# Optimization experiments

Hardware: AMD Instinct MI355X
Metric: run time of the kernel (lower is better)

The kernel has to match this reference:

```python
import jax, jax.numpy as jnp
import numpy as np

B, S, H = 2, 2048, 2048
N_HEADS = 16
HEAD_DIM = H // N_HEADS


def setup_inputs() -> dict:
    key = jax.random.key(0)
    k1, k2, k3 = jax.random.split(key, 3)
    # Xavier-uniform-ish init for weights, zeros for biases (matches _init_weights)
    lim_in = float(np.sqrt(6.0 / (H + 3 * H)))
    lim_out = float(np.sqrt(6.0 / (H + H)))
    return {
        "hidden_states": jax.random.normal(k1, (B, S, H), dtype=jnp.float32),
        "W_in": jax.random.uniform(k2, (3 * H, H), jnp.float32, -lim_in, lim_in),
        "b_in": jnp.zeros((3 * H,), jnp.float32),
        "W_out": jax.random.uniform(k3, (H, H), jnp.float32, -lim_out, lim_out),
        "b_out": jnp.zeros((H,), jnp.float32),
    }


def reference(hidden_states, W_in, b_in, W_out, b_out):
    b, s, h = hidden_states.shape
    qkv = hidden_states @ W_in.T + b_in  # [B,S,3H]
    q, k, v = jnp.split(qkv, 3, axis=-1)
    # [B,S,H] -> [B,N,S,D]
    def to_heads(x):
        return x.reshape(b, s, N_HEADS, HEAD_DIM).transpose(0, 2, 1, 3)
    q, k, v = to_heads(q), to_heads(k), to_heads(v)
    scale = HEAD_DIM ** -0.5
    scores = jnp.einsum("bnqd,bnkd->bnqk", q, k) * scale  # [B,N,S,S]
    causal = jnp.triu(jnp.ones((s, s), dtype=bool), k=1)
    scores = jnp.where(causal, -jnp.inf, scores)
    weights = jax.nn.softmax(scores, axis=-1)
    attn = jnp.einsum("bnqk,bnkd->bnqd", weights, v)  # [B,N,S,D]
    attn = attn.transpose(0, 2, 1, 3).reshape(b, s, h)
    return attn @ W_out.T + b_out
```

## Files before the change

### kernel.cpp

```cpp
#include <hip/hip_runtime.h>
#include <cstdint>

typedef __bf16 bf16x8 __attribute__((ext_vector_type(8)));
typedef __bf16 bf16x4 __attribute__((ext_vector_type(4)));
typedef float  f32x4  __attribute__((ext_vector_type(4)));

__device__ __forceinline__ void lds_load16(const void* g, void* l) {
  __builtin_amdgcn_global_load_lds(
      (const __attribute__((address_space(1))) unsigned int*)g,
      (__attribute__((address_space(3))) unsigned int*)l, 16, 0, 0);
}

#define BAR() do { asm volatile("" ::: "memory"); __builtin_amdgcn_s_barrier(); asm volatile("" ::: "memory"); } while (0)

__device__ __forceinline__ float grp16_max(float v) {
  v = fmaxf(v, __shfl_xor(v, 1));
  v = fmaxf(v, __shfl_xor(v, 2));
  v = fmaxf(v, __shfl_xor(v, 4));
  v = fmaxf(v, __shfl_xor(v, 8));
  return v;
}
__device__ __forceinline__ float grp16_sum(float v) {
  v += __shfl_xor(v, 1);
  v += __shfl_xor(v, 2);
  v += __shfl_xor(v, 4);
  v += __shfl_xor(v, 8);
  return v;
}

__global__ void f2bf_kernel(const float* __restrict__ in, __bf16* __restrict__ out, int n4) {
  int i = blockIdx.x * blockDim.x + threadIdx.x;
  if (i >= n4) return;
  const float4 v = reinterpret_cast<const float4*>(in)[i];
  bf16x4 o;
  o[0] = (__bf16)v.x; o[1] = (__bf16)v.y; o[2] = (__bf16)v.z; o[3] = (__bf16)v.w;
  reinterpret_cast<bf16x4*>(out)[i] = o;
}

template <int EPI>
__global__ __launch_bounds__(512, 1)
void gemm256(const __bf16* __restrict__ A, const __bf16* __restrict__ Bm,
             const float* __restrict__ bias,
             __bf16* __restrict__ qo, __bf16* __restrict__ ko, __bf16* __restrict__ vo,
             float* __restrict__ co)
{
  constexpr int K = 2048, NT = K / 64;
  __shared__ __align__(16) char lds8[131072];

  const int t = threadIdx.x;
  const int lane = t & 63, w = t >> 6;
  const int g = lane >> 4, r16 = lane & 15;
  const int wm = w >> 2, wn = w & 3;

  const int bid = blockIdx.x;
  int tM, tN;
  if (EPI == 0) {
    const int swz = (bid & 7) * 48 + (bid >> 3);
    tM = (swz & 15) * 256;
    tN = (swz >> 4) * 256;
  } else {
    const int swz = (bid & 7) * 16 + (bid >> 3);
    tM = (swz & 15) * 256;
    tN = (swz >> 4) * 256;
  }

  const char* Ag = (const char*)A + (size_t)tM * K * 2;
  const char* Bg = (const char*)Bm + (size_t)tN * K * 2;
  const int ld = K * 2;

  auto STAGE_HALF = [&](int X, int h, int tb, int ktg) {
#pragma unroll
    for (int i = 0; i < 2; i++) {
      int o = i * 8192 + t * 16;
      int rl = o >> 7;
      int inrow = (o & 127) ^ ((rl & 7) << 4);
      const char* src = (X ? Bg : Ag) + (size_t)(h * 128 + rl) * ld + (size_t)ktg * 128 + inrow;
      lds_load16(src, lds8 + tb * 65536 + X * 32768 + h * 16384 + o);
    }
  };

  const int xorv = (r16 & 7) << 4;
  const int aoff0 = (g * 16) ^ xorv;

  f32x4 acc[8][4] = {};
  bf16x8 af[8][2];
  bf16x8 bfm[2][2];

  STAGE_HALF(0, 0, 0, 0); STAGE_HALF(0, 1, 0, 0);
  STAGE_HALF(1, 0, 0, 0); STAGE_HALF(1, 1, 0, 0);
  STAGE_HALF(0, 0, 1, 1); STAGE_HALF(0, 1, 1, 1);
  asm volatile("s_waitcnt vmcnt(4)" ::: "memory");
  __builtin_amdgcn_s_barrier();

  for (int kt = 0; kt < NT; ++kt) {
    const int cb = kt & 1;
    const char* aT = lds8 + cb * 65536;
    const char* bT = aT + 32768;
    const int arow = (wm * 128 + r16) * 128;
    const int brow = (wn * 64 + r16) * 128;

#pragma unroll
    for (int mf = 0; mf < 4; mf++)
#pragma unroll
      for (int ks = 0; ks < 2; ks++)
        af[mf][ks] = *(const bf16x8*)(aT + arow + mf * 2048 + (aoff0 ^ (ks * 64)));
#pragma unroll
    for (int nf = 0; nf < 2; nf++)
#pragma unroll
      for (int ks = 0; ks < 2; ks++)
        bfm[nf][ks] = *(const bf16x8*)(bT + brow + nf * 2048 + (aoff0 ^ (ks * 64)));
    if (kt + 1 < NT) STAGE_HALF(1, 0, cb ^ 1, kt + 1);
    BAR();
    __builtin_amdgcn_s_setprio(1);
#pragma unroll
    for (int mf = 0; mf < 4; mf++)
#pragma unroll
      for (int nf = 0; nf < 2; nf++)
#pragma unroll
        for (int ks = 0; ks < 2; ks++)
          acc[mf][nf] = __builtin_amdgcn_mfma_f32_16x16x32_bf16(af[mf][ks], bfm[nf][ks], acc[mf][nf], 0, 0, 0);
    __builtin_amdgcn_s_setprio(0);
    BAR();

#pragma unroll
    for (int mf = 4; mf < 8; mf++)
#pragma unroll
      for (int ks = 0; ks < 2; ks++)
        af[mf][ks] = *(const bf16x8*)(aT + arow + mf * 2048 + (aoff0 ^ (ks * 64)));
#pragma unroll
    for (int nf = 0; nf < 2; nf++)
#pragma unroll
      for (int ks = 0; ks < 2; ks++)
        bfm[nf][ks] = *(const bf16x8*)(bT + brow + (nf + 2) * 2048 + (aoff0 ^ (ks * 64)));
    if (kt + 1 < NT) STAGE_HALF(1, 1, cb ^ 1, kt + 1);
    BAR();
    __builtin_amdgcn_s_setprio(1);
#pragma unroll
    for (int mf = 4; mf < 8; mf++)
#pragma unroll
      for (int nf = 0; nf < 2; nf++)
#pragma unroll
        for (int ks = 0; ks < 2; ks++)
          acc[mf][nf + 2] = __builtin_amdgcn_mfma_f32_16x16x32_bf16(af[mf][ks], bfm[nf][ks], acc[mf][nf + 2], 0, 0, 0);
    __builtin_amdgcn_s_setprio(0);
    BAR();

    if (kt + 2 < NT) STAGE_HALF(0, 0, cb, kt + 2);
    BAR();
    __builtin_amdgcn_s_setprio(1);
#pragma unroll
    for (int mf = 0; mf < 4; mf++)
#pragma unroll
      for (int nf = 0; nf < 2; nf++)
#pragma unroll
        for (int ks = 0; ks < 2; ks++)
          acc[mf][nf + 2] = __builtin_amdgcn_mfma_f32_16x16x32_bf16(af[mf][ks], bfm[nf][ks], acc[mf][nf + 2], 0, 0, 0);
    __builtin_amdgcn_s_setprio(0);
    BAR();

#pragma unroll
    for (int nf = 0; nf < 2; nf++)
#pragma unroll
      for (int ks = 0; ks < 2; ks++)
        bfm[nf][ks] = *(const bf16x8*)(bT + brow + nf * 2048 + (aoff0 ^ (ks * 64)));
    if (kt + 2 < NT) STAGE_HALF(0, 1, cb, kt + 2);
    BAR();
    __builtin_amdgcn_s_setprio(1);
#pragma unroll
    for (int mf = 4; mf < 8; mf++)
#pragma unroll
      for (int nf = 0; nf < 2; nf++)
#pragma unroll
        for (int ks = 0; ks < 2; ks++)
          acc[mf][nf] = __builtin_amdgcn_mfma_f32_16x16x32_bf16(af[mf][ks], bfm[nf][ks], acc[mf][nf], 0, 0, 0);
    __builtin_amdgcn_s_setprio(0);
    if (kt + 2 < NT) { asm volatile("s_waitcnt vmcnt(4)" ::: "memory"); }
    else             { asm volatile("s_waitcnt vmcnt(0)" ::: "memory"); }
    BAR();
  }

  if (EPI == 0) {
#pragma unroll
    for (int nf = 0; nf < 4; nf++) {
      int col = tN + wn * 64 + nf * 16 + r16;
      float bv = bias[col];
      int which = col >> 11;
      int f = col & 2047;
      int head = f >> 7, dd = f & 127;
      if (which == 2) {
#pragma unroll
        for (int mf = 0; mf < 8; mf++)
#pragma unroll
          for (int r = 0; r < 4; r++) {
            int m = tM + wm * 128 + mf * 16 + g * 4 + r;
            int bb2 = m >> 11, s = m & 2047;
            vo[((size_t)(bb2 * 16 + head) * 128 + dd) * 2048 + s] = (__bf16)(acc[mf][nf][r] + bv);
          }
      } else {
        __bf16* dst = (which == 0) ? qo : ko;
        float sc = (which == 0) ? 0.12751757f : 1.0f;
#pragma unroll
        for (int mf = 0; mf < 8; mf++)
#pragma unroll
          for (int r = 0; r < 4; r++) {
            int m = tM + wm * 128 + mf * 16 + g * 4 + r;
            int bb2 = m >> 11, s = m & 2047;
            dst[((size_t)(bb2 * 16 + head) * 2048 + s) * 128 + dd] = (__bf16)((acc[mf][nf][r] + bv) * sc);
          }
      }
    }
  } else {
    constexpr int N = 2048;
#pragma unroll
    for (int nf = 0; nf < 4; nf++) {
      int col = tN + wn * 64 + nf * 16 + r16;
      float bv = bias[col];
#pragma unroll
      for (int mf = 0; mf < 8; mf++)
#pragma unroll
        for (int r = 0; r < 4; r++) {
          int m = tM + wm * 128 + mf * 16 + g * 4 + r;
          co[(size_t)m * N + col] = acc[mf][nf][r] + bv;
        }
    }
  }
}

__global__ __launch_bounds__(256)
void attn_kernel(const __bf16* __restrict__ Qb, const __bf16* __restrict__ Kb,
                 const __bf16* __restrict__ Vb, __bf16* __restrict__ Ob)
{
  const int bid = blockIdx.x;
  const int qi = 31 - (bid >> 5);
  const int bh = bid & 31;
  const int b = bh >> 4, head = bh & 15;
  const int t = threadIdx.x, lane = t & 63, w = t >> 6;
  const int g = lane >> 4, r16 = lane & 15;

  __shared__ __align__(16) __bf16 Ks[64 * 128];
  __shared__ __align__(16) __bf16 Vs[128 * 64];
  __shared__ __align__(16) __bf16 Ps[4][16 * 72];

  const int q0 = qi * 64;
  const size_t hoff = (size_t)bh * 2048 * 128;
  const char* Kt0 = (const char*)(Kb + hoff);
  const char* Vt0 = (const char*)(Vb + hoff);

  bf16x8 qf[4];
  {
    const __bf16* qp = Qb + hoff + (size_t)(q0 + w * 16 + r16) * 128 + g * 8;
#pragma unroll
    for (int ks = 0; ks < 4; ks++) qf[ks] = *(const bf16x8*)(qp + ks * 32);
  }

  f32x4 oacc[8] = {};
  float m_run[4], l_run[4];
#pragma unroll
  for (int r = 0; r < 4; r++) { m_run[r] = -1e30f; l_run[r] = 0.f; }

  for (int kt = 0; kt <= qi; ++kt) {
#pragma unroll
    for (int it = 0; it < 4; it++) {
      int o = it * 4096 + t * 16;
      int swz = o ^ (((o >> 8) & 7) << 4);
      lds_load16(Kt0 + (size_t)kt * 16384 + swz, (char*)Ks + o);
    }
#pragma unroll
    for (int it = 0; it < 4; it++) {
      int o = it * 4096 + t * 16;
      int swz = o ^ (((o >> 7) & 7) << 4);
      lds_load16(Vt0 + (size_t)kt * 128 + (size_t)(swz >> 7) * 4096 + (swz & 127), (char*)Vs + o);
    }
    __syncthreads();

    f32x4 sf[4];
#pragma unroll
    for (int ni = 0; ni < 4; ni++) {
      f32x4 a = {};
#pragma unroll
      for (int ks = 0; ks < 4; ks++) {
        int row = ni * 16 + r16;
        int off = (row * 256 + (ks * 32 + g * 8) * 2) ^ ((row & 7) << 4);
        bf16x8 kf = *(const bf16x8*)((const char*)Ks + off);
        a = __builtin_amdgcn_mfma_f32_16x16x32_bf16(qf[ks], kf, a, 0, 0, 0);
      }
      sf[ni] = a;
    }

    if (kt == qi) {
#pragma unroll
      for (int ni = 0; ni < 4; ni++) {
        int kg = kt * 64 + ni * 16 + r16;
#pragma unroll
        for (int r = 0; r < 4; r++) {
          int qg = q0 + w * 16 + g * 4 + r;
          if (kg > qg) sf[ni][r] = -1e30f;
        }
      }
    }

#pragma unroll
    for (int r = 0; r < 4; r++) {
      float mx = fmaxf(fmaxf(sf[0][r], sf[1][r]), fmaxf(sf[2][r], sf[3][r]));
      mx = grp16_max(mx);
      float mn = fmaxf(m_run[r], mx);
      float alpha = __builtin_amdgcn_exp2f(m_run[r] - mn);
      float ps = 0.f;
#pragma unroll
      for (int ni = 0; ni < 4; ni++) {
        float p = __builtin_amdgcn_exp2f(sf[ni][r] - mn);
        sf[ni][r] = p; ps += p;
      }
      ps = grp16_sum(ps);
      l_run[r] = l_run[r] * alpha + ps;
      m_run[r] = mn;
#pragma unroll
      for (int di = 0; di < 8; di++) oacc[di][r] *= alpha;
    }

#pragma unroll
    for (int ni = 0; ni < 4; ni++)
#pragma unroll
      for (int r = 0; r < 4; r++)
        Ps[w][(g * 4 + r) * 72 + ni * 16 + r16] = (__bf16)sf[ni][r];

#pragma unroll
    for (int ks2 = 0; ks2 < 2; ks2++) {
      bf16x8 pa = *(const bf16x8*)&Ps[w][r16 * 72 + ks2 * 32 + g * 8];
#pragma unroll
      for (int di = 0; di < 8; di++) {
        int d_ = di * 16 + r16;
        int off = ((d_ << 7) + (ks2 * 32 + g * 8) * 2) ^ ((d_ & 7) << 4);
        bf16x8 vf = *(const bf16x8*)((const char*)Vs + off);
        oacc[di] = __builtin_amdgcn_mfma_f32_16x16x32_bf16(pa, vf, oacc[di], 0, 0, 0);
      }
    }
    __syncthreads();
  }

#pragma unroll
  for (int r = 0; r < 4; r++) {
    float inv = 1.0f / l_run[r];
    size_t rowb = ((size_t)b * 2048 + q0 + w * 16 + g * 4 + r) * 2048 + head * 128 + r16;
#pragma unroll
    for (int di = 0; di < 8; di++)
      Ob[rowb + di * 16] = (__bf16)(oacc[di][r] * inv);
  }
}

extern "C" void kernel_launch(void* const* d_in, const int* in_sizes, int n_in,
                              void* d_out, int out_size, void* d_ws, size_t ws_size,
                              hipStream_t stream) {
  const float* X  = (const float*)d_in[0];
  const float* Wi = (const float*)d_in[1];
  const float* bi = (const float*)d_in[2];
  const float* Wo = (const float*)d_in[3];
  const float* bo = (const float*)d_in[4];
  float* out = (float*)d_out;

  char* p = (char*)d_ws;
  auto alloc = [&](size_t bytes) {
    char* r = p;
    p += (bytes + 255) & ~(size_t)255;
    return r;
  };
  __bf16* Xb  = (__bf16*)alloc((size_t)4096 * 2048 * 2);
  __bf16* Wib = (__bf16*)alloc((size_t)6144 * 2048 * 2);
  __bf16* Wob = (__bf16*)alloc((size_t)2048 * 2048 * 2);
  __bf16* Qb  = (__bf16*)alloc((size_t)32 * 2048 * 128 * 2);
  __bf16* Kb  = (__bf16*)alloc((size_t)32 * 2048 * 128 * 2);
  __bf16* Vb  = (__bf16*)alloc((size_t)32 * 2048 * 128 * 2);
  __bf16* Ab  = (__bf16*)alloc((size_t)4096 * 2048 * 2);

  {
    int n4 = 4096 * 2048 / 4;
    f2bf_kernel<<<(n4 + 255) / 256, 256, 0, stream>>>(X, Xb, n4);
  }
  {
    int n4 = 6144 * 2048 / 4;
    f2bf_kernel<<<(n4 + 255) / 256, 256, 0, stream>>>(Wi, Wib, n4);
  }
  {
    int n4 = 2048 * 2048 / 4;
    f2bf_kernel<<<(n4 + 255) / 256, 256, 0, stream>>>(Wo, Wob, n4);
  }

  gemm256<0><<<dim3(384), 512, 0, stream>>>(Xb, Wib, bi, Qb, Kb, Vb, nullptr);
  attn_kernel<<<dim3(1024), 256, 0, stream>>>(Qb, Kb, Vb, Ab);
  gemm256<1><<<dim3(128), 512, 0, stream>>>(Ab, Wob, bo, nullptr, nullptr, nullptr, out);
}
```

Baseline: 415.3 us.

## Templatize GEMM tile width, use 256x128 tiles for output projection, restructure staging

Measured after the change: 412.2 us. No clear change (-0.7%).

```diff
diff --git a/kernel.cpp b/kernel.cpp
--- a/kernel.cpp
+++ b/kernel.cpp
@@ -37,7 +37,7 @@
   reinterpret_cast<bf16x4*>(out)[i] = o;
 }
 
-template <int EPI>
+template <int BN, int EPI>
 __global__ __launch_bounds__(512, 1)
 void gemm256(const __bf16* __restrict__ A, const __bf16* __restrict__ Bm,
              const float* __restrict__ bias,
@@ -45,7 +45,15 @@
              float* __restrict__ co)
 {
   constexpr int K = 2048, NT = K / 64;
-  __shared__ __align__(16) char lds8[131072];
+  constexpr int NF = BN / 64;
+  constexpr int NH = NF / 2;
+  constexpr int ABYTES = 32768;
+  constexpr int BBYTES = BN * 128;
+  constexpr int HB = BBYTES / 2;
+  constexpr int BUFB = ABYTES + BBYTES;
+  constexpr int BLOADS = BN / 128;
+  constexpr int LPT = 4 + 2 * BLOADS;
+  __shared__ __align__(16) char lds8[2 * BUFB];
 
   const int t = threadIdx.x;
   const int lane = t & 63, w = t >> 6;
@@ -59,129 +67,145 @@
     tM = (swz & 15) * 256;
     tN = (swz >> 4) * 256;
   } else {
-    const int swz = (bid & 7) * 16 + (bid >> 3);
+    const int swz = (bid & 7) * 32 + (bid >> 3);
     tM = (swz & 15) * 256;
-    tN = (swz >> 4) * 256;
+    tN = (swz >> 4) * BN;
   }
 
   const char* Ag = (const char*)A + (size_t)tM * K * 2;
   const char* Bg = (const char*)Bm + (size_t)tN * K * 2;
   const int ld = K * 2;
 
-  auto STAGE_HALF = [&](int X, int h, int tb, int ktg) {
+  auto STAGE_A = [&](int h, int tb, int ktg) {
 #pragma unroll
     for (int i = 0; i < 2; i++) {
       int o = i * 8192 + t * 16;
-      int rl = o >> 7;
-      int inrow = (o & 127) ^ ((rl & 7) << 4);
-      const char* src = (X ? Bg : Ag) + (size_t)(h * 128 + rl) * ld + (size_t)ktg * 128 + inrow;
-      lds_load16(src, lds8 + tb * 65536 + X * 32768 + h * 16384 + o);
+      int slot = o >> 11;
+      int row  = (o >> 7) & 15;
+      int inb  = (o & 127) ^ ((row & 7) << 4);
+      int grow = (slot >> 2) * 128 + (h * 4 + (slot & 3)) * 16 + row;
+      lds_load16(Ag + (size_t)grow * ld + (size_t)ktg * 128 + inb,
+                 lds8 + tb * BUFB + h * 16384 + o);
     }
   };
-
-  const int xorv = (r16 & 7) << 4;
-  const int aoff0 = (g * 16) ^ xorv;
-
-  f32x4 acc[8][4] = {};
-  bf16x8 af[8][2];
-  bf16x8 bfm[2][2];
-
-  STAGE_HALF(0, 0, 0, 0); STAGE_HALF(0, 1, 0, 0);
-  STAGE_HALF(1, 0, 0, 0); STAGE_HALF(1, 1, 0, 0);
-  STAGE_HALF(0, 0, 1, 1); STAGE_HALF(0, 1, 1, 1);
-  asm volatile("s_waitcnt vmcnt(4)" ::: "memory");
+  auto STAGE_B = [&](int h, int tb, int ktg) {
+#pragma unroll
+    for (int i = 0; i < BLOADS; i++) {
+      int o = i * 8192 + t * 16;
+      int slot = o >> 11;
+      int row  = (o >> 7) & 15;
+      int inb  = (o & 127) ^ ((row & 7) << 4);
+      int grow;
+      if (BN == 256) grow = (slot >> 1) * 64 + (h * 2 + (slot & 1)) * 16 + row;
+      else           grow = slot * 32 + h * 16 + row;
+      lds_load16(Bg + (size_t)grow * ld + (size_t)ktg * 128 + inb,
+                 lds8 + tb * BUFB + ABYTES + h * HB + o);
+    }
+  };
+
+  const int inA = (g * 16) ^ ((r16 & 7) << 4);
+  const int rbase = r16 * 128;
+
+  f32x4 acc[8][NF] = {};
+  bf16x8 af0[4][2], af1[4][2];
+  bf16x8 bfm[NF][2];
+
+  STAGE_A(0, 0, 0); STAGE_A(1, 0, 0); STAGE_B(0, 0, 0); STAGE_B(1, 0, 0);
+  STAGE_A(0, 1, 1); STAGE_A(1, 1, 1); STAGE_B(0, 1, 1); STAGE_B(1, 1, 1);
+  if (LPT == 8) { asm volatile("s_waitcnt vmcnt(8)" ::: "memory"); }
+  else          { asm volatile("s_waitcnt vmcnt(6)" ::: "memory"); }
   __builtin_amdgcn_s_barrier();
 
   for (int kt = 0; kt < NT; ++kt) {
     const int cb = kt & 1;
-    const char* aT = lds8 + cb * 65536;
-    const char* bT = aT + 32768;
-    const int arow = (wm * 128 + r16) * 128;
-    const int brow = (wn * 64 + r16) * 128;
-
-#pragma unroll
-    for (int mf = 0; mf < 4; mf++)
+    const char* aT = lds8 + cb * BUFB;
+    const char* bT = aT + ABYTES;
+
+#pragma unroll
+    for (int mq = 0; mq < 4; mq++)
 #pragma unroll
       for (int ks = 0; ks < 2; ks++)
-        af[mf][ks] = *(const bf16x8*)(aT + arow + mf * 2048 + (aoff0 ^ (ks * 64)));
-#pragma unroll
-    for (int nf = 0; nf < 2; nf++)
+        af0[mq][ks] = *(const bf16x8*)(aT + (wm * 4 + mq) * 2048 + rbase + (inA ^ (ks * 64)));
+#pragma unroll
+    for (int nf = 0; nf < NH; nf++) {
+      int slot = (BN == 256) ? (wn * 2 + nf) : wn;
 #pragma unroll
       for (int ks = 0; ks < 2; ks++)
-        bfm[nf][ks] = *(const bf16x8*)(bT + brow + nf * 2048 + (aoff0 ^ (ks * 64)));
-    if (kt + 1 < NT) STAGE_HALF(1, 0, cb ^ 1, kt + 1);
+        bfm[nf][ks] = *(const bf16x8*)(bT + slot * 2048 + rbase + (inA ^ (ks * 64)));
+    }
     BAR();
     __builtin_amdgcn_s_setprio(1);
 #pragma unroll
-    for (int mf = 0; mf < 4; mf++)
-#pragma unroll
-      for (int nf = 0; nf < 2; nf++)
+    for (int mq = 0; mq < 4; mq++)
+#pragma unroll
+      for (int nf = 0; nf < NH; nf++)
 #pragma unroll
         for (int ks = 0; ks < 2; ks++)
-          acc[mf][nf] = __builtin_amdgcn_mfma_f32_16x16x32_bf16(af[mf][ks], bfm[nf][ks], acc[mf][nf], 0, 0, 0);
+          acc[mq][nf] = __builtin_amdgcn_mfma_f32_16x16x32_bf16(af0[mq][ks], bfm[nf][ks], acc[mq][nf], 0, 0, 0);
     __builtin_amdgcn_s_setprio(0);
     BAR();
 
 #pragma unroll
-    for (int mf = 4; mf < 8; mf++)
+    for (int nf = NH; nf < NF; nf++) {
+      int slot = (BN == 256) ? (wn * 2 + (nf & 1)) : wn;
 #pragma unroll
       for (int ks = 0; ks < 2; ks++)
-        af[mf][ks] = *(const bf16x8*)(aT + arow + mf * 2048 + (aoff0 ^ (ks * 64)));
-#pragma unroll
-    for (int nf = 0; nf < 2; nf++)
+        bfm[nf][ks] = *(const bf16x8*)(bT + HB + slot * 2048 + rbase + (inA ^ (ks * 64)));
+    }
+    if (kt + 2 < NT) STAGE_B(0, cb, kt + 2);
+    BAR();
+    __builtin_amdgcn_s_setprio(1);
+#pragma unroll
+    for (int mq = 0; mq < 4; mq++)
+#pragma unroll
+      for (int nf = NH; nf < NF; nf++)
+#pragma unroll
+        for (int ks = 0; ks < 2; ks++)
+          acc[mq][nf] = __builtin_amdgcn_mfma_f32_16x16x32_bf16(af0[mq][ks], bfm[nf][ks], acc[mq][nf], 0, 0, 0);
+    __builtin_amdgcn_s_setprio(0);
+    BAR();
+
+#pragma unroll
+    for (int mq = 0; mq < 4; mq++)
 #pragma unroll
       for (int ks = 0; ks < 2; ks++)
-        bfm[nf][ks] = *(const bf16x8*)(bT + brow + (nf + 2) * 2048 + (aoff0 ^ (ks * 64)));
-    if (kt + 1 < NT) STAGE_HALF(1, 1, cb ^ 1, kt + 1);
+        af1[mq][ks] = *(const bf16x8*)(aT + 16384 + (wm * 4 + mq) * 2048 + rbase + (inA ^ (ks * 64)));
+    if (kt + 2 < NT) { STAGE_A(0, cb, kt + 2); STAGE_B(1, cb, kt + 2); }
     BAR();
     __builtin_amdgcn_s_setprio(1);
 #pragma unroll
-    for (int mf = 4; mf < 8; mf++)
-#pragma unroll
-      for (int nf = 0; nf < 2; nf++)
+    for (int mq = 0; mq < 4; mq++)
+#pragma unroll
+      for (int nf = 0; nf < NH; nf++)
 #pragma unroll
         for (int ks = 0; ks < 2; ks++)
-          acc[mf][nf + 2] = __builtin_amdgcn_mfma_f32_16x16x32_bf16(af[mf][ks], bfm[nf][ks], acc[mf][nf + 2], 0, 0, 0);
+          acc[mq + 4][nf] = __builtin_amdgcn_mfma_f32_16x16x32_bf16(af1[mq][ks], bfm[nf][ks], acc[mq + 4][nf], 0, 0, 0);
     __builtin_amdgcn_s_setprio(0);
     BAR();
 
-    if (kt + 2 < NT) STAGE_HALF(0, 0, cb, kt + 2);
+    if (kt + 2 < NT) STAGE_A(1, cb, kt + 2);
     BAR();
     __builtin_amdgcn_s_setprio(1);
 #pragma unroll
-    for (int mf = 0; mf < 4; mf++)
-#pragma unroll
-      for (int nf = 0; nf < 2; nf++)
+    for (int mq = 0; mq < 4; mq++)
+#pragma unroll
+      for (int nf = NH; nf < NF; nf++)
 #pragma unroll
         for (int ks = 0; ks < 2; ks++)
-          acc[mf][nf + 2] = __builtin_amdgcn_mfma_f32_16x16x32_bf16(af[mf][ks], bfm[nf][ks], acc[mf][nf + 2], 0, 0, 0);
+          acc[mq + 4][nf] = __builtin_amdgcn_mfma_f32_16x16x32_bf16(af1[mq][ks], bfm[nf][ks], acc[mq + 4][nf], 0, 0, 0);
     __builtin_amdgcn_s_setprio(0);
-    BAR();
-
-#pragma unroll
-    for (int nf = 0; nf < 2; nf++)
-#pragma unroll
-      for (int ks = 0; ks < 2; ks++)
-        bfm[nf][ks] = *(const bf16x8*)(bT + brow + nf * 2048 + (aoff0 ^ (ks * 64)));
-    if (kt + 2 < NT) STAGE_HALF(0, 1, cb, kt + 2);
-    BAR();
-    __builtin_amdgcn_s_setprio(1);
-#pragma unroll
-    for (int mf = 4; mf < 8; mf++)
-#pragma unroll
-      for (int nf = 0; nf < 2; nf++)
-#pragma unroll
-        for (int ks = 0; ks < 2; ks++)
-          acc[mf][nf] = __builtin_amdgcn_mfma_f32_16x16x32_bf16(af[mf][ks], bfm[nf][ks], acc[mf][nf], 0, 0, 0);
-    __builtin_amdgcn_s_setprio(0);
-    if (kt + 2 < NT) { asm volatile("s_waitcnt vmcnt(4)" ::: "memory"); }
-    else             { asm volatile("s_waitcnt vmcnt(0)" ::: "memory"); }
+    if (kt + 2 < NT) {
+      if (LPT == 8) { asm volatile("s_waitcnt vmcnt(8)" ::: "memory"); }
+      else          { asm volatile("s_waitcnt vmcnt(6)" ::: "memory"); }
+    } else {
+      asm volatile("s_waitcnt vmcnt(0)" ::: "memory");
+    }
     BAR();
   }
 
   if (EPI == 0) {
 #pragma unroll
-    for (int nf = 0; nf < 4; nf++) {
+    for (int nf = 0; nf < NF; nf++) {
       int col = tN + wn * 64 + nf * 16 + r16;
       float bv = bias[col];
       int which = col >> 11;
@@ -212,8 +236,8 @@
   } else {
     constexpr int N = 2048;
 #pragma unroll
-    for (int nf = 0; nf < 4; nf++) {
-      int col = tN + wn * 64 + nf * 16 + r16;
+    for (int nf = 0; nf < NF; nf++) {
+      int col = tN + wn * (BN / 4) + nf * 16 + r16;
       float bv = bias[col];
 #pragma unroll
       for (int mf = 0; mf < 8; mf++)
@@ -385,7 +409,7 @@
     f2bf_kernel<<<(n4 + 255) / 256, 256, 0, stream>>>(Wo, Wob, n4);
   }
 
-  gemm256<0><<<dim3(384), 512, 0, stream>>>(Xb, Wib, bi, Qb, Kb, Vb, nullptr);
+  gemm256<256, 0><<<dim3(384), 512, 0, stream>>>(Xb, Wib, bi, Qb, Kb, Vb, nullptr);
   attn_kernel<<<dim3(1024), 256, 0, stream>>>(Qb, Kb, Vb, Ab);
-  gemm256<1><<<dim3(128), 512, 0, stream>>>(Ab, Wob, bo, nullptr, nullptr, nullptr, out);
-}
+  gemm256<128, 1><<<dim3(256), 512, 0, stream>>>(Ab, Wob, bo, nullptr, nullptr, nullptr, out);
+}
```
